# Optimization experiments

Hardware: AMD Instinct MI355X
Metric: run time of the kernel (lower is better)

Reference implementation:

```python
import jax, jax.numpy as jnp
import numpy as np

N, F_IN, F_OUT, H = 4096, 128, 64, 8
NEG_SLOPE = 0.2

def leaky_relu(x):
    return jnp.where(x >= 0, x, NEG_SLOPE * x)

def setup_inputs() -> dict:
    key = jax.random.key(0)
    k = jax.random.split(key, 6)
    x = jax.random.normal(k[0], (N, F_IN), dtype=jnp.float32)
    conn = jax.random.uniform(k[1], (N, N)) < 0.1
    conn = conn | jnp.eye(N, dtype=bool)
    topology = jnp.where(conn, 0.0, -1e9).astype(jnp.float32)
    proj = jax.random.normal(k[2], (H, F_IN, F_OUT), dtype=jnp.float32) * (1.0 / np.sqrt(F_IN))
    score_src = jax.random.normal(k[3], (H, F_OUT), dtype=jnp.float32) * (1.0 / np.sqrt(F_OUT))
    score_dst = jax.random.normal(k[4], (H, F_OUT), dtype=jnp.float32) * (1.0 / np.sqrt(F_OUT))
    skip_w = jax.random.normal(k[5], (H * F_OUT, F_IN), dtype=jnp.float32) * (1.0 / np.sqrt(F_IN))
    return {"x": x, "topology": topology, "proj": proj,
            "score_src": score_src, "score_dst": score_dst, "skip_w": skip_w}

def reference(x, topology, proj, score_src, score_dst, skip_w):
    # dropout is identity at inference time
    # projected node features: [H, N, F_OUT]
    h = jnp.einsum('ni,hio->hno', x, proj)
    # additive attention scores (GAT): [H, N, 1] + [H, 1, N] -> [H, N, N]
    s_src = jnp.einsum('hno,ho->hn', h, score_src)
    s_dst = jnp.einsum('hno,ho->hn', h, score_dst)
    scores = leaky_relu(s_src[:, :, None] + s_dst[:, None, :])
    attn = jax.nn.softmax(scores + topology[None, :, :], axis=-1)  # [H, N, N]
    # aggregate neighbors, then transpose heads to [N, H, F_OUT]
    out = jnp.einsum('hij,hjo->iho', attn, h)
    # skip connection (F_OUT != F_IN -> projected skip)
    out = out + (x @ skip_w.T).reshape(N, H, F_OUT)
    # mean over heads (concat_heads=False), then LeakyReLU activation
    out = leaky_relu(jnp.mean(out, axis=1))  # [N, F_OUT]
    return out
```

## Files before the change

### kernel.cpp

```cpp
#include <hip/hip_runtime.h>
#include <hip/hip_bf16.h>

#define NN 4096
#define FIN 128
#define FOUT 64
#define NH 8
#define KS 4
#define QT 32

typedef float f32x4 __attribute__((ext_vector_type(4)));
typedef __bf16 bf16x8 __attribute__((ext_vector_type(8)));
typedef unsigned long long u64;

__global__ __launch_bounds__(256) void maskwc_kernel(
    const float* __restrict__ topo, u64* __restrict__ mb,
    const float* __restrict__ proj, const float* __restrict__ score_src,
    const float* __restrict__ score_dst, const float* __restrict__ skip_w,
    float* __restrict__ Wc) {
    const int tid = threadIdx.x;
    if (blockIdx.x < 2048) {
        const int w = blockIdx.x * 4 + (tid >> 6);
        const int lane = tid & 63;
        size_t base = (size_t)w * 32;
#pragma unroll 4
        for (int it = 0; it < 32; ++it) {
            size_t u = base + it;
            float t = topo[u * 64 + lane];
            u64 b = __ballot(t > -0.5e9f);
            if (lane == 0) mb[u] = b;
        }
        return;
    }
    int idx = (blockIdx.x - 2048) * 256 + tid;
    if (idx >= FIN * 80) return;
    int i = idx / 80, c = idx % 80;
    float v = 0.f;
    if (c < 16) {
        int h = c & 7;
        const float* w = (c < 8 ? score_src : score_dst) + h * FOUT;
        const float* p = proj + (size_t)h * FIN * FOUT + (size_t)i * FOUT;
        for (int f = 0; f < FOUT; ++f) v += p[f] * w[f];
    } else {
        int f = c - 16;
        for (int h = 0; h < NH; ++h) v += skip_w[(size_t)(h * FOUT + f) * FIN + i];
        v *= 0.125f;
    }
    Wc[i * 80 + c] = v;
}

__global__ __launch_bounds__(256) void scores_kernel(
    const float* __restrict__ x, const float* __restrict__ Wc,
    float* __restrict__ skipm, unsigned* __restrict__ EF, float2* __restrict__ C12,
    __hip_bfloat16* __restrict__ xb_) {
    __shared__ float wcs[FIN][80];
    __shared__ float xs[16][FIN + 5];
    const int n0 = blockIdx.x * 16;
    const int tid = threadIdx.x;
    for (int i = tid; i < FIN * 80 / 4; i += 256)
        ((float4*)&wcs[0][0])[i] = ((const float4*)Wc)[i];
    const float4* xsrc = (const float4*)(x + (size_t)n0 * FIN);
    for (int i = tid; i < 16 * FIN / 4; i += 256) {
        int r = i >> 5, c4 = i & 31;
        *(float4*)&xs[r][c4 * 4] = xsrc[i];
    }
    __syncthreads();
    const int r = tid & 15;
    const int g = tid >> 4;
    float acc[4];
    float sa = 0.f;
#pragma unroll
    for (int j = 0; j < 4; ++j) acc[j] = 0.f;
#pragma unroll 4
    for (int i = 0; i < FIN; ++i) {
        float xv = xs[r][i];
        float4 p = *(float4*)&wcs[i][16 + g * 4];
        float qv = wcs[i][g];
        acc[0] += xv * p.x; acc[1] += xv * p.y; acc[2] += xv * p.z; acc[3] += xv * p.w;
        sa += xv * qv;
    }
    int n = n0 + r;
#pragma unroll
    for (int j = 0; j < 4; ++j) skipm[(size_t)n * FOUT + g * 4 + j] = acc[j];
    if (g < 8) {
        C12[g * NN + n] = make_float2(expf(sa), expf(0.2f * sa));
    } else {
        __hip_bfloat16 e0 = __float2bfloat16(expf(sa));
        __hip_bfloat16 f0 = __float2bfloat16(expf(0.2f * sa));
        EF[(g - 8) * NN + n] = ((unsigned)*(unsigned short*)&f0 << 16) | (unsigned)*(unsigned short*)&e0;
    }
    {
        int row = tid >> 4, col0 = (tid & 15) * 8;
        const float* src = &xs[row][col0];
        bf16x8 b0;
#pragma unroll
        for (int j = 0; j < 8; ++j) b0[j] = (__bf16)src[j];
        *(bf16x8*)((__bf16*)xb_ + (size_t)(n0 + row) * FIN + col0) = b0;
    }
}

__global__ __launch_bounds__(256) void vt_kernel(
    const float* __restrict__ proj, const __hip_bfloat16* __restrict__ xb_,
    __hip_bfloat16* __restrict__ Vt_) {
    __shared__ __bf16 pT[FOUT][FIN + 8];
    const int tid = threadIdx.x;
    const int h = blockIdx.x >> 6;
    const int ng = blockIdx.x & 63;
    const __bf16* xb = (const __bf16*)xb_;
    __bf16* Vt = (__bf16*)Vt_;
    for (int idx = tid; idx < FIN * FOUT; idx += 256) {
        int i = idx >> 6, f = idx & 63;
        pT[f][i] = (__bf16)proj[(size_t)h * FIN * FOUT + idx];
    }
    __syncthreads();
    const int wave = tid >> 6, lane = tid & 63, q = lane >> 4, li = lane & 15;
    const int nb = ng * 64 + wave * 16;
    f32x4 acc[4];
#pragma unroll
    for (int n = 0; n < 4; ++n) acc[n] = (f32x4){0.f, 0.f, 0.f, 0.f};
#pragma unroll
    for (int kt = 0; kt < 4; ++kt) {
        bf16x8 bfrag = *(const bf16x8*)(xb + (size_t)(nb + li) * FIN + kt * 32 + q * 8);
#pragma unroll
        for (int ft = 0; ft < 4; ++ft) {
            bf16x8 afrag = *(const bf16x8*)&pT[ft * 16 + li][kt * 32 + q * 8];
            acc[ft] = __builtin_amdgcn_mfma_f32_16x16x32_bf16(afrag, bfrag, acc[ft], 0, 0, 0);
        }
    }
#pragma unroll
    for (int ft = 0; ft < 4; ++ft)
#pragma unroll
        for (int reg = 0; reg < 4; ++reg)
            Vt[((size_t)h * FOUT + ft * 16 + q * 4 + reg) * NN + nb + li] = (__bf16)acc[ft][reg];
}

__attribute__((amdgpu_waves_per_eu(4)))
__global__ __launch_bounds__(256) void attn_kernel(
    const u64* __restrict__ maskbits, const __hip_bfloat16* __restrict__ Vt_,
    const unsigned* __restrict__ EFg, const float2* __restrict__ C12g,
    __hip_bfloat16* __restrict__ accP, float* __restrict__ rsP) {
    __shared__ u64 maskS[QT][17];
    __shared__ char vA[4][4096];
    __shared__ char vB[4][4096];
    const int tid = threadIdx.x;
    const int w = tid >> 6;
    const int lane = tid & 63, q = lane >> 4, li = lane & 15;
    const int qt = blockIdx.x >> 3, ks = (blockIdx.x >> 1) & 3, hb = blockIdx.x & 1;
    const int h = hb * 4 + w;
    const int row0 = qt * QT;
    const int kb0 = ks * 1024;

    const int r_ = lane >> 2;
    const int sg = ((lane & 3) - (r_ >> 1)) & 3;
    const size_t laneoff = (size_t)r_ * NN + sg * 8;
    const int rdoff = li * 64 + ((q + (li >> 1)) & 3) * 16;

    const __bf16* vb = (const __bf16*)Vt_ + (size_t)h * (FOUT * NN) + kb0;
    const unsigned* efb = EFg + (size_t)h * NN + kb0;

#define DMA_TILE(DST, KT) do {                                                     \
    _Pragma("unroll")                                                              \
    for (int c = 0; c < 4; ++c) {                                                  \
        const __bf16* g_ = vb + (size_t)c * (16 * NN) + (KT) * 32 + laneoff;       \
        __builtin_amdgcn_global_load_lds(                                          \
            (const __attribute__((address_space(1))) void*)g_,                     \
            (__attribute__((address_space(3))) void*)&DST[w][c * 1024], 16, 0, 0); \
    }                                                                              \
} while (0)

    DMA_TILE(vA, 0);
    {
        int i0 = tid, i1 = tid + 256;
        maskS[i0 >> 4][i0 & 15] = maskbits[(size_t)(row0 + (i0 >> 4)) * 64 + ks * 16 + (i0 & 15)];
        maskS[i1 >> 4][i1 & 15] = maskbits[(size_t)(row0 + (i1 >> 4)) * 64 + ks * 16 + (i1 & 15)];
    }
    __syncthreads();

    float C1[2], C2[2];
#pragma unroll
    for (int rt = 0; rt < 2; ++rt) {
        float2 c = C12g[(size_t)h * NN + row0 + rt * 16 + li];
        C1[rt] = c.x; C2[rt] = c.y;
    }
    bf16x8 ones;
#pragma unroll
    for (int j = 0; j < 8; ++j) ones[j] = (__bf16)1.0f;

    f32x4 acc[2][4];
    f32x4 rsacc[2];
#pragma unroll
    for (int rt = 0; rt < 2; ++rt) {
#pragma unroll
        for (int n = 0; n < 4; ++n) acc[rt][n] = (f32x4){0.f, 0.f, 0.f, 0.f};
        rsacc[rt] = (f32x4){0.f, 0.f, 0.f, 0.f};
    }

#define CHUNK_BODY(SRC, DSTN, KT) do {                                                        \
    const unsigned* ep_ = efb + (KT) * 32 + q * 8;                                            \
    uint4 ea_ = *(const uint4*)ep_;                                                           \
    uint4 eb_ = *(const uint4*)(ep_ + 4);                                                     \
    asm volatile("" ::: "memory");                           \
    DMA_TILE(DSTN, ((KT) + 1) & 31);                                                          \
    asm volatile("s_waitcnt vmcnt(4)" ::: "memory");                                          \
    bf16x8 vf_[4];                                                                            \
    _Pragma("unroll")                                                                         \
    for (int n = 0; n < 4; ++n)                                                               \
        vf_[n] = *(const bf16x8*)&SRC[w][n * 1024 + rdoff];                                   \
    unsigned ew_[8] = {ea_.x, ea_.y, ea_.z, ea_.w, eb_.x, eb_.y, eb_.z, eb_.w};               \
    _Pragma("unroll")                                                                         \
    for (int rt = 0; rt < 2; ++rt) {                                                          \
        u64 mw_ = maskS[rt * 16 + li][(KT) >> 1];                                             \
        unsigned mm_ = (unsigned)(mw_ >> (((KT) & 1) * 32 + q * 8)) & 0xffu;                  \
        bf16x8 pf_;                                                                           \
        _Pragma("unroll")                                                                     \
        for (int j = 0; j < 8; ++j) {                                                         \
            unsigned e_ = ew_[j];                                                             \
            float E_ = __uint_as_float(e_ << 16);                                             \
            float F_ = __uint_as_float(e_ & 0xffff0000u);                                     \
            float pv_ = fmaxf(C1[rt] * E_, C2[rt] * F_);                                      \
            pv_ = ((mm_ >> j) & 1u) ? pv_ : 0.f;                                              \
            pf_[j] = (__bf16)pv_;                                                             \
        }                                                                                     \
        rsacc[rt] = __builtin_amdgcn_mfma_f32_16x16x32_bf16(pf_, ones, rsacc[rt], 0, 0, 0);   \
        _Pragma("unroll")                                                                     \
        for (int n = 0; n < 4; ++n)                                                           \
            acc[rt][n] = __builtin_amdgcn_mfma_f32_16x16x32_bf16(pf_, vf_[n], acc[rt][n],     \
                                                                 0, 0, 0);                    \
    }                                                                                         \
} while (0)

#pragma unroll 1
    for (int kt = 0; kt < 32; kt += 2) {
        CHUNK_BODY(vA, vB, kt);
        CHUNK_BODY(vB, vA, kt + 1);
    }
#undef CHUNK_BODY
#undef DMA_TILE

#pragma unroll
    for (int rt = 0; rt < 2; ++rt) {
        if (li == 0) {
#pragma unroll
            for (int reg = 0; reg < 4; ++reg)
                rsP[(size_t)(ks * NH + h) * NN + row0 + rt * 16 + q * 4 + reg] = rsacc[rt][reg];
        }
        __hip_bfloat16* ap = accP + ((size_t)(ks * NH + h) * NN + row0 + rt * 16) * 64;
#pragma unroll
        for (int n = 0; n < 4; ++n)
#pragma unroll
            for (int reg = 0; reg < 4; ++reg)
                ap[(q * 4 + reg) * 64 + n * 16 + li] = __float2bfloat16(acc[rt][n][reg]);
    }
}

__global__ __launch_bounds__(256) void combine_kernel(
    const __hip_bfloat16* __restrict__ accP, const float* __restrict__ rsP,
    float* __restrict__ out) {
    int idx = blockIdx.x * 256 + threadIdx.x;
    int row = idx >> 6, f = idx & 63;
    float s = 0.f;
#pragma unroll 1
    for (int h = 0; h < NH; ++h) {
        float a = 0.f, r = 0.f;
#pragma unroll
        for (int k = 0; k < KS; ++k) {
            a += __bfloat162float(accP[((size_t)(k * NH + h) * NN + row) * 64 + f]);
            r += rsP[(size_t)(k * NH + h) * NN + row];
        }
        s += a / r;
    }
    float v = s * 0.125f + out[idx];
    out[idx] = fmaxf(v, 0.2f * v);
}

extern "C" void kernel_launch(void* const* d_in, const int* in_sizes, int n_in,
                              void* d_out, int out_size, void* d_ws, size_t ws_size,
                              hipStream_t stream) {
    (void)in_sizes; (void)n_in; (void)out_size; (void)ws_size;
    const float* x         = (const float*)d_in[0];
    const float* topology  = (const float*)d_in[1];
    const float* proj      = (const float*)d_in[2];
    const float* score_src = (const float*)d_in[3];
    const float* score_dst = (const float*)d_in[4];
    const float* skip_w    = (const float*)d_in[5];
    float* out = (float*)d_out;

    char* ws = (char*)d_ws;
    __hip_bfloat16* xb = (__hip_bfloat16*)ws;
    __hip_bfloat16* Vt = (__hip_bfloat16*)(ws + 1048576);
    unsigned* EF  = (unsigned*)(ws + 5242880);
    float2* C12   = (float2*)(ws + 5373952);
    float* Wc     = (float*)(ws + 5636096);
    u64* maskbits = (u64*)(ws + 5677056);
    float* rsP    = (float*)(ws + 7774208);
    __hip_bfloat16* accP = (__hip_bfloat16*)(ws + 8298496);
    float* skipm = out;

    maskwc_kernel<<<2088, 256, 0, stream>>>(topology, maskbits, proj, score_src,
                                            score_dst, skip_w, Wc);
    scores_kernel<<<256, 256, 0, stream>>>(x, Wc, skipm, EF, C12, xb);
    vt_kernel<<<512, 256, 0, stream>>>(proj, xb, Vt);
    attn_kernel<<<1024, 256, 0, stream>>>(maskbits, Vt, EF, C12, accP, rsP);
    combine_kernel<<<1024, 256, 0, stream>>>(accP, rsP, out);
}
```

Measured before the change: 184.4 us.

## Switch attention probabilities to fp16 packed math with bitmask-to-bytemask expansion

Changes the intermediate precision from bf16 to fp16 for x, V, and the exponentiated scores. The probability computation in the attention inner loop now uses packed half2 multiplies and max instead of per-element fp32 math with bf16 conversion. The adjacency mask bits are expanded into per-half masks with multiply and perm tricks and applied with a bitwise AND instead of selects. The row constants are pre-scaled by 1/8 to keep fp16 in range. This risks fp16 overflow or underflow in the exp terms and products.

```diff
diff --git a/kernel.cpp b/kernel.cpp
--- a/kernel.cpp
+++ b/kernel.cpp
@@ -9,8 +9,12 @@
 #define QT 32
 
 typedef float f32x4 __attribute__((ext_vector_type(4)));
-typedef __bf16 bf16x8 __attribute__((ext_vector_type(8)));
+typedef _Float16 f16x8 __attribute__((ext_vector_type(8)));
+typedef _Float16 h2 __attribute__((ext_vector_type(2)));
 typedef unsigned long long u64;
+
+static __device__ __forceinline__ h2 as_h2(unsigned u) { return __builtin_bit_cast(h2, u); }
+static __device__ __forceinline__ unsigned as_u32(h2 v) { return __builtin_bit_cast(unsigned, v); }
 
 __global__ __launch_bounds__(256) void maskwc_kernel(
     const float* __restrict__ topo, u64* __restrict__ mb,
@@ -50,8 +54,8 @@
 
 __global__ __launch_bounds__(256) void scores_kernel(
     const float* __restrict__ x, const float* __restrict__ Wc,
-    float* __restrict__ skipm, unsigned* __restrict__ EF, float2* __restrict__ C12,
-    __hip_bfloat16* __restrict__ xb_) {
+    float* __restrict__ skipm, _Float16* __restrict__ Eh, _Float16* __restrict__ Fh,
+    unsigned* __restrict__ Cc, _Float16* __restrict__ xb) {
     __shared__ float wcs[FIN][80];
     __shared__ float xs[16][FIN + 5];
     const int n0 = blockIdx.x * 16;
@@ -82,34 +86,36 @@
 #pragma unroll
     for (int j = 0; j < 4; ++j) skipm[(size_t)n * FOUT + g * 4 + j] = acc[j];
     if (g < 8) {
-        C12[g * NN + n] = make_float2(expf(sa), expf(0.2f * sa));
+        _Float16 c1 = (_Float16)(expf(sa) * 0.125f);
+        _Float16 c2 = (_Float16)(expf(0.2f * sa) * 0.125f);
+        unsigned short u1 = __builtin_bit_cast(unsigned short, c1);
+        unsigned short u2 = __builtin_bit_cast(unsigned short, c2);
+        Cc[(size_t)g * NN + n] = ((unsigned)u2 << 16) | (unsigned)u1;
     } else {
-        __hip_bfloat16 e0 = __float2bfloat16(expf(sa));
-        __hip_bfloat16 f0 = __float2bfloat16(expf(0.2f * sa));
-        EF[(g - 8) * NN + n] = ((unsigned)*(unsigned short*)&f0 << 16) | (unsigned)*(unsigned short*)&e0;
+        int h = g - 8;
+        Eh[(size_t)h * NN + n] = (_Float16)expf(sa);
+        Fh[(size_t)h * NN + n] = (_Float16)expf(0.2f * sa);
     }
     {
         int row = tid >> 4, col0 = (tid & 15) * 8;
         const float* src = &xs[row][col0];
-        bf16x8 b0;
-#pragma unroll
-        for (int j = 0; j < 8; ++j) b0[j] = (__bf16)src[j];
-        *(bf16x8*)((__bf16*)xb_ + (size_t)(n0 + row) * FIN + col0) = b0;
+        f16x8 b0;
+#pragma unroll
+        for (int j = 0; j < 8; ++j) b0[j] = (_Float16)src[j];
+        *(f16x8*)(xb + (size_t)(n0 + row) * FIN + col0) = b0;
     }
 }
 
 __global__ __launch_bounds__(256) void vt_kernel(
-    const float* __restrict__ proj, const __hip_bfloat16* __restrict__ xb_,
-    __hip_bfloat16* __restrict__ Vt_) {
-    __shared__ __bf16 pT[FOUT][FIN + 8];
+    const float* __restrict__ proj, const _Float16* __restrict__ xb,
+    _Float16* __restrict__ Vt) {
+    __shared__ _Float16 pT[FOUT][FIN + 8];
     const int tid = threadIdx.x;
     const int h = blockIdx.x >> 6;
     const int ng = blockIdx.x & 63;
-    const __bf16* xb = (const __bf16*)xb_;
-    __bf16* Vt = (__bf16*)Vt_;
     for (int idx = tid; idx < FIN * FOUT; idx += 256) {
         int i = idx >> 6, f = idx & 63;
-        pT[f][i] = (__bf16)proj[(size_t)h * FIN * FOUT + idx];
+        pT[f][i] = (_Float16)proj[(size_t)h * FIN * FOUT + idx];
     }
     __syncthreads();
     const int wave = tid >> 6, lane = tid & 63, q = lane >> 4, li = lane & 15;
@@ -119,24 +125,25 @@
     for (int n = 0; n < 4; ++n) acc[n] = (f32x4){0.f, 0.f, 0.f, 0.f};
 #pragma unroll
     for (int kt = 0; kt < 4; ++kt) {
-        bf16x8 bfrag = *(const bf16x8*)(xb + (size_t)(nb + li) * FIN + kt * 32 + q * 8);
+        f16x8 bfrag = *(const f16x8*)(xb + (size_t)(nb + li) * FIN + kt * 32 + q * 8);
 #pragma unroll
         for (int ft = 0; ft < 4; ++ft) {
-            bf16x8 afrag = *(const bf16x8*)&pT[ft * 16 + li][kt * 32 + q * 8];
-            acc[ft] = __builtin_amdgcn_mfma_f32_16x16x32_bf16(afrag, bfrag, acc[ft], 0, 0, 0);
+            f16x8 afrag = *(const f16x8*)&pT[ft * 16 + li][kt * 32 + q * 8];
+            acc[ft] = __builtin_amdgcn_mfma_f32_16x16x32_f16(afrag, bfrag, acc[ft], 0, 0, 0);
         }
     }
 #pragma unroll
     for (int ft = 0; ft < 4; ++ft)
 #pragma unroll
         for (int reg = 0; reg < 4; ++reg)
-            Vt[((size_t)h * FOUT + ft * 16 + q * 4 + reg) * NN + nb + li] = (__bf16)acc[ft][reg];
+            Vt[((size_t)h * FOUT + ft * 16 + q * 4 + reg) * NN + nb + li] = (_Float16)acc[ft][reg];
 }
 
 __attribute__((amdgpu_waves_per_eu(4)))
 __global__ __launch_bounds__(256) void attn_kernel(
-    const u64* __restrict__ maskbits, const __hip_bfloat16* __restrict__ Vt_,
-    const unsigned* __restrict__ EFg, const float2* __restrict__ C12g,
+    const u64* __restrict__ maskbits, const _Float16* __restrict__ Vtg,
+    const _Float16* __restrict__ Ehg, const _Float16* __restrict__ Fhg,
+    const unsigned* __restrict__ Ccg,
     __hip_bfloat16* __restrict__ accP, float* __restrict__ rsP) {
     __shared__ u64 maskS[QT][17];
     __shared__ char vA[4][4096];
@@ -154,13 +161,14 @@
     const size_t laneoff = (size_t)r_ * NN + sg * 8;
     const int rdoff = li * 64 + ((q + (li >> 1)) & 3) * 16;
 
-    const __bf16* vb = (const __bf16*)Vt_ + (size_t)h * (FOUT * NN) + kb0;
-    const unsigned* efb = EFg + (size_t)h * NN + kb0;
+    const _Float16* vb = Vtg + (size_t)h * (FOUT * NN) + kb0;
+    const _Float16* Ehq = Ehg + (size_t)h * NN + kb0 + q * 8;
+    const _Float16* Fhq = Fhg + (size_t)h * NN + kb0 + q * 8;
 
 #define DMA_TILE(DST, KT) do {                                                     \
     _Pragma("unroll")                                                              \
     for (int c = 0; c < 4; ++c) {                                                  \
-        const __bf16* g_ = vb + (size_t)c * (16 * NN) + (KT) * 32 + laneoff;       \
+        const _Float16* g_ = vb + (size_t)c * (16 * NN) + (KT) * 32 + laneoff;     \
         __builtin_amdgcn_global_load_lds(                                          \
             (const __attribute__((address_space(1))) void*)g_,                     \
             (__attribute__((address_space(3))) void*)&DST[w][c * 1024], 16, 0, 0); \
@@ -175,15 +183,16 @@
     }
     __syncthreads();
 
-    float C1[2], C2[2];
+    h2 c1h[2], c2h[2];
 #pragma unroll
     for (int rt = 0; rt < 2; ++rt) {
-        float2 c = C12g[(size_t)h * NN + row0 + rt * 16 + li];
-        C1[rt] = c.x; C2[rt] = c.y;
-    }
-    bf16x8 ones;
-#pragma unroll
-    for (int j = 0; j < 8; ++j) ones[j] = (__bf16)1.0f;
+        unsigned cw = Ccg[(size_t)h * NN + row0 + rt * 16 + li];
+        c1h[rt] = as_h2((cw << 16) | (cw & 0xffffu));
+        c2h[rt] = as_h2((cw >> 16) | (cw & 0xffff0000u));
+    }
+    f16x8 ones;
+#pragma unroll
+    for (int j = 0; j < 8; ++j) ones[j] = (_Float16)1.0f;
 
     f32x4 acc[2][4];
     f32x4 rsacc[2];
@@ -195,36 +204,41 @@
     }
 
 #define CHUNK_BODY(SRC, DSTN, KT) do {                                                        \
-    const unsigned* ep_ = efb + (KT) * 32 + q * 8;                                            \
-    uint4 ea_ = *(const uint4*)ep_;                                                           \
-    uint4 eb_ = *(const uint4*)(ep_ + 4);                                                     \
-    asm volatile("" ::: "memory");                           \
+    uint4 ea_ = *(const uint4*)(Ehq + (KT) * 32);                                             \
+    uint4 fa_ = *(const uint4*)(Fhq + (KT) * 32);                                             \
+    asm volatile("" ::: "memory");                          \
     DMA_TILE(DSTN, ((KT) + 1) & 31);                                                          \
     asm volatile("s_waitcnt vmcnt(4)" ::: "memory");                                          \
-    bf16x8 vf_[4];                                                                            \
+    f16x8 vf_[4];                                                                             \
     _Pragma("unroll")                                                                         \
     for (int n = 0; n < 4; ++n)                                                               \
-        vf_[n] = *(const bf16x8*)&SRC[w][n * 1024 + rdoff];                                   \
-    unsigned ew_[8] = {ea_.x, ea_.y, ea_.z, ea_.w, eb_.x, eb_.y, eb_.z, eb_.w};               \
+        vf_[n] = *(const f16x8*)&SRC[w][n * 1024 + rdoff];                                    \
+    unsigned ew_[4] = {ea_.x, ea_.y, ea_.z, ea_.w};                                           \
+    unsigned fw_[4] = {fa_.x, fa_.y, fa_.z, fa_.w};                                           \
     _Pragma("unroll")                                                                         \
     for (int rt = 0; rt < 2; ++rt) {                                                          \
         u64 mw_ = maskS[rt * 16 + li][(KT) >> 1];                                             \
         unsigned mm_ = (unsigned)(mw_ >> (((KT) & 1) * 32 + q * 8)) & 0xffu;                  \
-        bf16x8 pf_;                                                                           \
+        unsigned blo_ = ((mm_ & 0xFu) * 0x204081u) & 0x01010101u;                             \
+        unsigned bhi_ = ((mm_ >> 4) * 0x204081u) & 0x01010101u;                               \
+        blo_ *= 0xFFu; bhi_ *= 0xFFu;                                                         \
+        unsigned mk_[4] = {__builtin_amdgcn_perm(0u, blo_, 0x01010000u),                      \
+                           __builtin_amdgcn_perm(0u, blo_, 0x03030202u),                      \
+                           __builtin_amdgcn_perm(0u, bhi_, 0x01010000u),                      \
+                           __builtin_amdgcn_perm(0u, bhi_, 0x03030202u)};                     \
+        union { f16x8 v; unsigned u[4]; } pf_;                                                \
         _Pragma("unroll")                                                                     \
-        for (int j = 0; j < 8; ++j) {                                                         \
-            unsigned e_ = ew_[j];                                                             \
-            float E_ = __uint_as_float(e_ << 16);                                             \
-            float F_ = __uint_as_float(e_ & 0xffff0000u);                                     \
-            float pv_ = fmaxf(C1[rt] * E_, C2[rt] * F_);                                      \
-            pv_ = ((mm_ >> j) & 1u) ? pv_ : 0.f;                                              \
-            pf_[j] = (__bf16)pv_;                                                             \
+        for (int j2 = 0; j2 < 4; ++j2) {                                                      \
+            h2 t_ = c1h[rt] * as_h2(ew_[j2]);                                                 \
+            h2 u_ = c2h[rt] * as_h2(fw_[j2]);                                                 \
+            h2 p_ = __builtin_elementwise_max(t_, u_);                                        \
+            pf_.u[j2] = as_u32(p_) & mk_[j2];                                                 \
         }                                                                                     \
-        rsacc[rt] = __builtin_amdgcn_mfma_f32_16x16x32_bf16(pf_, ones, rsacc[rt], 0, 0, 0);   \
+        rsacc[rt] = __builtin_amdgcn_mfma_f32_16x16x32_f16(pf_.v, ones, rsacc[rt], 0, 0, 0);  \
         _Pragma("unroll")                                                                     \
         for (int n = 0; n < 4; ++n)                                                           \
-            acc[rt][n] = __builtin_amdgcn_mfma_f32_16x16x32_bf16(pf_, vf_[n], acc[rt][n],     \
-                                                                 0, 0, 0);                    \
+            acc[rt][n] = __builtin_amdgcn_mfma_f32_16x16x32_f16(pf_.v, vf_[n], acc[rt][n],    \
+                                                                0, 0, 0);                     \
     }                                                                                         \
 } while (0)
 
@@ -285,20 +299,21 @@
     float* out = (float*)d_out;
 
     char* ws = (char*)d_ws;
-    __hip_bfloat16* xb = (__hip_bfloat16*)ws;
-    __hip_bfloat16* Vt = (__hip_bfloat16*)(ws + 1048576);
-    unsigned* EF  = (unsigned*)(ws + 5242880);
-    float2* C12   = (float2*)(ws + 5373952);
-    float* Wc     = (float*)(ws + 5636096);
-    u64* maskbits = (u64*)(ws + 5677056);
-    float* rsP    = (float*)(ws + 7774208);
-    __hip_bfloat16* accP = (__hip_bfloat16*)(ws + 8298496);
+    _Float16* xb   = (_Float16*)ws;
+    _Float16* Vt   = (_Float16*)(ws + 1048576);
+    _Float16* Eh   = (_Float16*)(ws + 5242880);
+    _Float16* Fh   = (_Float16*)(ws + 5308416);
+    unsigned* Cc   = (unsigned*)(ws + 5373952);
+    float* Wc      = (float*)(ws + 5505024);
+    u64* maskbits  = (u64*)(ws + 5545984);
+    float* rsP     = (float*)(ws + 7643136);
+    __hip_bfloat16* accP = (__hip_bfloat16*)(ws + 8167424);
     float* skipm = out;
 
     maskwc_kernel<<<2088, 256, 0, stream>>>(topology, maskbits, proj, score_src,
                                             score_dst, skip_w, Wc);
-    scores_kernel<<<256, 256, 0, stream>>>(x, Wc, skipm, EF, C12, xb);
+    scores_kernel<<<256, 256, 0, stream>>>(x, Wc, skipm, Eh, Fh, Cc, xb);
     vt_kernel<<<512, 256, 0, stream>>>(proj, xb, Vt);
-    attn_kernel<<<1024, 256, 0, stream>>>(maskbits, Vt, EF, C12, accP, rsP);
+    attn_kernel<<<1024, 256, 0, stream>>>(maskbits, Vt, Eh, Fh, Cc, accP, rsP);
     combine_kernel<<<1024, 256, 0, stream>>>(accP, rsP, out);
 }
```

Result: faster. 179.2 us (-2.8%).
